# Kernel tuning notes

Measured on AMD Instinct MI355X. Metric: run time of the kernel, lower is better.

The kernel has to match this reference:

```python
import jax, jax.numpy as jnp
import numpy as np

H, W = 512, 512
N_GAUSS = 4096
T_EPS = 1e-3          # early-termination threshold from the torch loop
COV_DIAG = 25.0       # hardcoded cov_2d = eye(2) * 25 in rasterize_gaussians


def quat_to_rot(q):
    # standard (w, x, y, z) quaternion -> rotation matrix, with normalization
    q = q / jnp.linalg.norm(q)
    w, x, y, z = q[0], q[1], q[2], q[3]
    return jnp.array([
        [1 - 2 * (y * y + z * z), 2 * (x * y - w * z),     2 * (x * z + w * y)],
        [2 * (x * y + w * z),     1 - 2 * (x * x + z * z), 2 * (y * z - w * x)],
        [2 * (x * z - w * y),     2 * (y * z + w * x),     1 - 2 * (x * x + y * y)],
    ])


def setup_inputs() -> dict:
    key = jax.random.key(0)
    k0, k1, k2, k3 = jax.random.split(key, 4)
    xy = jax.random.uniform(k0, (N_GAUSS, 2), minval=-2.0, maxval=2.0)
    z = jax.random.uniform(k1, (N_GAUSS, 1), minval=4.0, maxval=10.0)
    positions = jnp.concatenate([xy, z], axis=-1)                    # [N,3], z>0
    colors = jax.random.uniform(k2, (N_GAUSS, 3))                    # [N,3] in [0,1]
    opacities = jax.random.uniform(k3, (N_GAUSS,)) * 0.5             # [N]
    quaternion = jnp.array([1.0, 0.05, 0.02, 0.01], dtype=jnp.float32)
    cam_position = jnp.zeros(3, dtype=jnp.float32)
    intrinsics = jnp.array([[500.0, 0.0, 256.0],
                            [0.0, 500.0, 256.0],
                            [0.0, 0.0, 1.0]], dtype=jnp.float32)
    background_color = jnp.zeros(3, dtype=jnp.float32)
    return {"positions": positions, "colors": colors, "opacities": opacities,
            "quaternion": quaternion, "cam_position": cam_position,
            "intrinsics": intrinsics, "background_color": background_color}


def _render(positions, colors, opacities, quaternion, cam_position, intrinsics,
            background_color):
    R = quat_to_rot(quaternion)                                      # [3,3]
    pos_cam = (positions - cam_position[None, :]) @ R.T              # [N,3]
    proj = pos_cam @ intrinsics.T                                    # [N,3]
    screen = proj[:, :2] / proj[:, 2:3]                              # [N,2]
    depths = proj[:, 2]                                              # [N]

    order = jnp.argsort(-depths)                                     # back-to-front
    centers_s = screen[order]
    colors_s = colors[order]
    opac_s = opacities[order]
    depth_s = pos_cam[order, 2]

    yy, xx = jnp.meshgrid(jnp.arange(H, dtype=jnp.float32),
                          jnp.arange(W, dtype=jnp.float32), indexing="ij")
    pix = jnp.stack([xx, yy], axis=-1)                               # [H,W,2] (x,y)

    init_color = jnp.broadcast_to(background_color[:, None, None], (3, H, W))
    carry0 = (init_color, jnp.zeros((H, W)), jnp.zeros((H, W)), jnp.ones((H, W)))

    def step(carry, g):
        color_acc, depth_acc, alpha_acc, T = carry
        center, color, opacity, depth = g
        # emulate the `if transmittance.max() < 1e-3: break` exactly: once T
        # saturates it is monotone, so masking all later contributions == break
        active = (jnp.max(T) >= T_EPS).astype(T.dtype)
        diff = pix - center[None, None, :]                           # [H,W,2]
        mahal = jnp.sum(diff * diff, axis=-1) / COV_DIAG             # cov_inv = I/25
        alpha = jnp.clip(jnp.exp(-0.5 * mahal) * opacity, 0.0, 1.0) * active
        ta = T * alpha
        color_acc = color_acc + ta[None, :, :] * color[:, None, None]
        depth_acc = depth_acc + ta * depth
        alpha_acc = alpha_acc + ta
        T = T * (1.0 - alpha)
        return (color_acc, depth_acc, alpha_acc, T), None

    (image, depth_map, alpha_map, _), _ = jax.lax.scan(
        step, carry0, (centers_s, colors_s, opac_s, depth_s))
    return image, depth_map, alpha_map


def reference(positions, colors, opacities, quaternion, cam_position, intrinsics,
              background_color):
    return _render(positions, colors, opacities, quaternion, cam_position,
                   intrinsics, background_color)
```

## Files before the change

kernel.cpp:

```cpp
#include <hip/hip_runtime.h>
#include <hip/hip_bf16.h>

#define N_GAUSS 4096
#define H 512
#define W 512
#define HW (H * W)


__global__ void proj_kernel(const float* __restrict__ pos,
                            const float* __restrict__ quat,
                            const float* __restrict__ cam,
                            const float* __restrict__ K,
                            float* __restrict__ cx, float* __restrict__ cy,
                            float* __restrict__ dz, float* __restrict__ key,
                            int* __restrict__ rank) {
    int i = blockIdx.x * blockDim.x + threadIdx.x;
    if (i >= N_GAUSS) return;
    float qw = quat[0], qx = quat[1], qy = quat[2], qz = quat[3];
    float qn = 1.0f / sqrtf(qw * qw + qx * qx + qy * qy + qz * qz);
    qw *= qn; qx *= qn; qy *= qn; qz *= qn;
    float r00 = 1.f - 2.f * (qy * qy + qz * qz), r01 = 2.f * (qx * qy - qw * qz), r02 = 2.f * (qx * qz + qw * qy);
    float r10 = 2.f * (qx * qy + qw * qz), r11 = 1.f - 2.f * (qx * qx + qz * qz), r12 = 2.f * (qy * qz - qw * qx);
    float r20 = 2.f * (qx * qz - qw * qy), r21 = 2.f * (qy * qz + qw * qx), r22 = 1.f - 2.f * (qx * qx + qy * qy);
    float px = pos[3 * i] - cam[0], py = pos[3 * i + 1] - cam[1], pz = pos[3 * i + 2] - cam[2];
    float X = r00 * px + r01 * py + r02 * pz;
    float Y = r10 * px + r11 * py + r12 * pz;
    float Z = r20 * px + r21 * py + r22 * pz;
    float u = K[0] * X + K[1] * Y + K[2] * Z;
    float v = K[3] * X + K[4] * Y + K[5] * Z;
    float w = K[6] * X + K[7] * Y + K[8] * Z;
    cx[i] = u / w;
    cy[i] = v / w;
    dz[i] = Z;
    key[i] = -w;
    rank[i] = 0;
}

__global__ __launch_bounds__(256) void rank_partial_kernel(
        const float* __restrict__ keyg, int* __restrict__ rank) {
    __shared__ __align__(16) float sk[256];
    int t = threadIdx.x;
    int jbase = blockIdx.y * 256;
    sk[t] = keyg[jbase + t];
    __syncthreads();
    int i = blockIdx.x * 256 + t;
    float ki = keyg[i];
    int r = 0;
    #pragma unroll
    for (int j = 0; j < 256; j += 4) {
        float4 k4 = *reinterpret_cast<const float4*>(&sk[j]);
        r += (k4.x < ki) || (k4.x == ki && (jbase + j + 0) < i);
        r += (k4.y < ki) || (k4.y == ki && (jbase + j + 1) < i);
        r += (k4.z < ki) || (k4.z == ki && (jbase + j + 2) < i);
        r += (k4.w < ki) || (k4.w == ki && (jbase + j + 3) < i);
    }
    if (r) atomicAdd(&rank[i], r);
}

__global__ __launch_bounds__(256) void scatter_kernel(
        const int* __restrict__ rank, const float* __restrict__ cx,
        const float* __restrict__ cy, const float* __restrict__ dz,
        const float* __restrict__ colors, const float* __restrict__ opac,
        float4* __restrict__ out) {
    int i = blockIdx.x * 256 + threadIdx.x;
    int r = rank[i];
    out[2 * r]     = make_float4(cx[i], cy[i], dz[i], opac[i]);
    out[2 * r + 1] = make_float4(colors[3 * i], colors[3 * i + 1], colors[3 * i + 2], 0.f);
}

#define CHUNK 256
#define CULL2 1444.0f

__global__ __launch_bounds__(256) void render_kernel(
        const float4* __restrict__ gs, const float* __restrict__ bg,
        float* __restrict__ out) {
    __shared__ float4 cmp[2 * CHUNK];
    __shared__ unsigned long long wmask[4];
    __shared__ int walive[4];
    int tx = threadIdx.x, ty = threadIdx.y;
    int tid = ty * 16 + tx;
    int lane = tid & 63, wid = tid >> 6;
    int j = blockIdx.x * 16 + tx;
    int i = blockIdx.y * 16 + ty;
    float px = (float)j, py = (float)i;
    float tcx = blockIdx.x * 16 + 7.5f, tcy = blockIdx.y * 16 + 7.5f;
    float T = 1.f;
    float cr = bg[0], cg = bg[1], cb = bg[2];
    float da = 0.f, aa = 0.f;
    for (int c0 = 0; c0 < N_GAUSS; c0 += CHUNK) {
        float4 A = gs[2 * (c0 + tid)];
        float4 C = gs[2 * (c0 + tid) + 1];
        float ddx = A.x - tcx, ddy = A.y - tcy;
        bool pred = (ddx * ddx + ddy * ddy <= CULL2);
        unsigned long long m = __ballot(pred ? 1 : 0);
        unsigned long long am = __ballot(T >= 1e-6f ? 1 : 0);
        if (lane == 0) { wmask[wid] = m; walive[wid] = (am != 0ull); }
        __syncthreads();
        if (!(walive[0] | walive[1] | walive[2] | walive[3])) break;
        unsigned long long m0 = wmask[0], m1 = wmask[1], m2 = wmask[2], m3 = wmask[3];
        int total = __popcll(m0) + __popcll(m1) + __popcll(m2) + __popcll(m3);
        if (pred) {
            int base = 0;
            if (wid > 0) base += __popcll(m0);
            if (wid > 1) base += __popcll(m1);
            if (wid > 2) base += __popcll(m2);
            int pos = base + __popcll(m & ((1ull << lane) - 1ull));
            cmp[2 * pos]     = A;
            cmp[2 * pos + 1] = C;
        }
        __syncthreads();
        for (int g = 0; g < total; ++g) {
            float4 GA = cmp[2 * g];
            float dx = px - GA.x, dy = py - GA.y;
            float al = __expf(-0.02f * (dx * dx + dy * dy)) * GA.w;
            float ta = T * al;
            float4 GC = cmp[2 * g + 1];
            cr += ta * GC.x; cg += ta * GC.y; cb += ta * GC.z;
            da += ta * GA.z; aa += ta;
            T -= ta;
        }
        __syncthreads();
    }
    int pid = i * W + j;
    out[pid]          = cr;
    out[HW + pid]     = cg;
    out[2 * HW + pid] = cb;
    out[3 * HW + pid] = da;
    out[4 * HW + pid] = aa;
}

extern "C" void kernel_launch(void* const* d_in, const int* in_sizes, int n_in,
                              void* d_out, int out_size, void* d_ws, size_t ws_size,
                              hipStream_t stream) {
    const float* positions = (const float*)d_in[0];
    const float* colors    = (const float*)d_in[1];
    const float* opacities = (const float*)d_in[2];
    const float* quat      = (const float*)d_in[3];
    const float* cam       = (const float*)d_in[4];
    const float* intr      = (const float*)d_in[5];
    const float* bg        = (const float*)d_in[6];
    float* out = (float*)d_out;

    float* ws  = (float*)d_ws;
    float* cx  = ws;
    float* cy  = ws + 4096;
    float* dz  = ws + 8192;
    float* key = ws + 12288;
    int*   rank = (int*)(ws + 16384);
    float4* sorted = (float4*)(ws + 20480);

    proj_kernel<<<dim3(N_GAUSS / 256), dim3(256), 0, stream>>>(
        positions, quat, cam, intr, cx, cy, dz, key, rank);
    rank_partial_kernel<<<dim3(16, 16), dim3(256), 0, stream>>>(key, rank);
    scatter_kernel<<<dim3(N_GAUSS / 256), dim3(256), 0, stream>>>(
        rank, cx, cy, dz, colors, opacities, sorted);
    render_kernel<<<dim3(W / 16, H / 16), dim3(16, 16), 0, stream>>>(
        sorted, bg, out);
}
```

Measured before the change: 116.2 us.

## Pre-cull all gaussians per tile up front and render in compacted batches

Scatter now also writes a compact float2 center array. Each render block first culls all 4096 gaussians against its tile from that lighter array and builds a compacted index list with ballots and a prefix scan. It then loads only the surviving gaussians in batches of up to 512. This removes the per-chunk reload of full 32-byte records and the barriers per 256-gaussian chunk. Saturation checks move into the inner loop every 128 gaussians, tiles are launched in a permuted order to spread load, and the change uses much more shared memory, which may lower occupancy.

Measured after the change: 126.9 us. +9.2%, slower.

```diff
diff --git a/kernel.cpp b/kernel.cpp
--- a/kernel.cpp
+++ b/kernel.cpp
@@ -61,55 +61,87 @@
         const int* __restrict__ rank, const float* __restrict__ cx,
         const float* __restrict__ cy, const float* __restrict__ dz,
         const float* __restrict__ colors, const float* __restrict__ opac,
-        float4* __restrict__ out) {
+        float4* __restrict__ out, float2* __restrict__ cxy) {
     int i = blockIdx.x * 256 + threadIdx.x;
     int r = rank[i];
-    out[2 * r]     = make_float4(cx[i], cy[i], dz[i], opac[i]);
+    float x = cx[i], y = cy[i];
+    out[2 * r]     = make_float4(x, y, dz[i], opac[i]);
     out[2 * r + 1] = make_float4(colors[3 * i], colors[3 * i + 1], colors[3 * i + 2], 0.f);
-}
-
-#define CHUNK 256
+    cxy[r] = make_float2(x, y);
+}
+
 #define CULL2 1444.0f
+#define NSUB 64
+#define CAP 512
 
 __global__ __launch_bounds__(256) void render_kernel(
-        const float4* __restrict__ gs, const float* __restrict__ bg,
-        float* __restrict__ out) {
-    __shared__ float4 cmp[2 * CHUNK];
-    __shared__ unsigned long long wmask[4];
-    __shared__ int walive[4];
-    int tx = threadIdx.x, ty = threadIdx.y;
-    int tid = ty * 16 + tx;
+        const float4* __restrict__ gs, const float2* __restrict__ cxy,
+        const float* __restrict__ bg, float* __restrict__ out) {
+    __shared__ unsigned long long smask[NSUB];
+    __shared__ int sprefix[NSUB + 1];
+    __shared__ unsigned short sidx[N_GAUSS];
+    __shared__ __align__(16) float4 cmp[2 * CAP];
+    __shared__ int swalive[4];
+
+    int tid = threadIdx.x;
     int lane = tid & 63, wid = tid >> 6;
-    int j = blockIdx.x * 16 + tx;
-    int i = blockIdx.y * 16 + ty;
+    int tile = (blockIdx.x * 341) & 1023;
+    int tx0 = (tile & 31) * 16, ty0 = (tile >> 5) * 16;
+    int j = tx0 + (tid & 15);
+    int i = ty0 + (tid >> 4);
     float px = (float)j, py = (float)i;
-    float tcx = blockIdx.x * 16 + 7.5f, tcy = blockIdx.y * 16 + 7.5f;
+    float tcx = tx0 + 7.5f, tcy = ty0 + 7.5f;
+
+    for (int k = 0; k < 16; ++k) {
+        int sc = k * 4 + wid;
+        int g = sc * 64 + lane;
+        float2 c2 = cxy[g];
+        float ddx = c2.x - tcx, ddy = c2.y - tcy;
+        bool pred = (ddx * ddx + ddy * ddy <= CULL2);
+        unsigned long long m = __ballot(pred ? 1 : 0);
+        if (pred) {
+            int pos = __popcll(m & ((1ull << lane) - 1ull));
+            sidx[sc * 64 + pos] = (unsigned short)g;
+        }
+        if (lane == 0) smask[sc] = m;
+    }
+    __syncthreads();
+
+    if (wid == 0) {
+        int c = __popcll(smask[lane]);
+        int inc = c;
+        #pragma unroll
+        for (int d = 1; d < 64; d <<= 1) {
+            int n = __shfl_up(inc, d, 64);
+            if (lane >= d) inc += n;
+        }
+        sprefix[lane] = inc - c;
+        if (lane == 63) sprefix[64] = inc;
+    }
+    __syncthreads();
+    int total = sprefix[64];
+
     float T = 1.f;
     float cr = bg[0], cg = bg[1], cb = bg[2];
     float da = 0.f, aa = 0.f;
-    for (int c0 = 0; c0 < N_GAUSS; c0 += CHUNK) {
-        float4 A = gs[2 * (c0 + tid)];
-        float4 C = gs[2 * (c0 + tid) + 1];
-        float ddx = A.x - tcx, ddy = A.y - tcy;
-        bool pred = (ddx * ddx + ddy * ddy <= CULL2);
-        unsigned long long m = __ballot(pred ? 1 : 0);
-        unsigned long long am = __ballot(T >= 1e-6f ? 1 : 0);
-        if (lane == 0) { wmask[wid] = m; walive[wid] = (am != 0ull); }
+    bool saturated = false;
+
+    for (int base = 0; base < total && !saturated; base += CAP) {
+        int cnt = min(CAP, total - base);
+        for (int s = tid; s < cnt; s += 256) {
+            int gpos = base + s;
+            int lo = 0, hi = NSUB;
+            #pragma unroll
+            for (int it = 0; it < 6; ++it) {
+                int mid = (lo + hi) >> 1;
+                if (sprefix[mid] <= gpos) lo = mid; else hi = mid;
+            }
+            int idx = sidx[lo * 64 + (gpos - sprefix[lo])];
+            cmp[2 * s]     = gs[2 * idx];
+            cmp[2 * s + 1] = gs[2 * idx + 1];
+        }
         __syncthreads();
-        if (!(walive[0] | walive[1] | walive[2] | walive[3])) break;
-        unsigned long long m0 = wmask[0], m1 = wmask[1], m2 = wmask[2], m3 = wmask[3];
-        int total = __popcll(m0) + __popcll(m1) + __popcll(m2) + __popcll(m3);
-        if (pred) {
-            int base = 0;
-            if (wid > 0) base += __popcll(m0);
-            if (wid > 1) base += __popcll(m1);
-            if (wid > 2) base += __popcll(m2);
-            int pos = base + __popcll(m & ((1ull << lane) - 1ull));
-            cmp[2 * pos]     = A;
-            cmp[2 * pos + 1] = C;
-        }
-        __syncthreads();
-        for (int g = 0; g < total; ++g) {
+        for (int g = 0; g < cnt; ++g) {
             float4 GA = cmp[2 * g];
             float dx = px - GA.x, dy = py - GA.y;
             float al = __expf(-0.02f * (dx * dx + dy * dy)) * GA.w;
@@ -118,9 +150,18 @@
             cr += ta * GC.x; cg += ta * GC.y; cb += ta * GC.z;
             da += ta * GA.z; aa += ta;
             T -= ta;
+            if ((g & 127) == 127 && g + 1 < cnt) {
+                unsigned long long alive = __ballot(T >= 1e-6f ? 1 : 0);
+                if (lane == 0) swalive[wid] = (alive != 0ull);
+                __syncthreads();
+                bool allsat = !(swalive[0] | swalive[1] | swalive[2] | swalive[3]);
+                __syncthreads();
+                if (allsat) { saturated = true; break; }
+            }
         }
         __syncthreads();
     }
+
     int pid = i * W + j;
     out[pid]          = cr;
     out[HW + pid]     = cg;
@@ -148,12 +189,13 @@
     float* key = ws + 12288;
     int*   rank = (int*)(ws + 16384);
     float4* sorted = (float4*)(ws + 20480);
+    float2* cxy    = (float2*)(ws + 53248);
 
     proj_kernel<<<dim3(N_GAUSS / 256), dim3(256), 0, stream>>>(
         positions, quat, cam, intr, cx, cy, dz, key, rank);
     rank_partial_kernel<<<dim3(16, 16), dim3(256), 0, stream>>>(key, rank);
     scatter_kernel<<<dim3(N_GAUSS / 256), dim3(256), 0, stream>>>(
-        rank, cx, cy, dz, colors, opacities, sorted);
-    render_kernel<<<dim3(W / 16, H / 16), dim3(16, 16), 0, stream>>>(
-        sorted, bg, out);
-}
+        rank, cx, cy, dz, colors, opacities, sorted, cxy);
+    render_kernel<<<dim3(W / 16 * H / 16), dim3(256), 0, stream>>>(
+        sorted, cxy, bg, out);
+}
```
